# Kernel optimization log

Measured on AMD Instinct MI355X. Metric: run time of the kernel, lower is better.

Reference implementation:

```python
import jax, jax.numpy as jnp
import numpy as np
import math

B, S, HID = 2, 2048, 2048
NH, NKV, HD = 16, 4, 128
ROPE_BASE = 10000.0

def _rope(x, position_ids):
    # x: [B, H, S, HD], position_ids: [B, S]
    half = HD // 2
    inv_freq = 1.0 / (ROPE_BASE ** (jnp.arange(0, half, dtype=jnp.float32) / half))
    freqs = position_ids.astype(jnp.float32)[:, :, None] * inv_freq[None, None, :]  # [B,S,half]
    cos = jnp.cos(freqs)[:, None, :, :]  # [B,1,S,half]
    sin = jnp.sin(freqs)[:, None, :, :]
    x1, x2 = x[..., :half], x[..., half:]
    return jnp.concatenate([x1 * cos - x2 * sin, x2 * cos + x1 * sin], axis=-1)

def setup_inputs() -> dict:
    key = jax.random.key(0)
    k1, k2, k3 = jax.random.split(key, 3)
    x = jax.random.normal(k1, (B, S, HID), dtype=jnp.float32)
    position_ids = jnp.broadcast_to(jnp.arange(S, dtype=jnp.int64 if jax.config.jax_enable_x64 else jnp.int32)[None, :], (B, S))
    causal = jnp.tril(jnp.ones((S, S), dtype=bool))
    mask = jnp.where(causal, 0.0, -1e9).astype(jnp.float32)[None, None, :, :]
    w_qkv = jax.random.normal(k2, (NH * HD + 2 * NKV * HD, HID), dtype=jnp.float32) * 0.02
    w_o = jax.random.normal(k3, (HID, HID), dtype=jnp.float32) * 0.02
    return {"x": x, "position_ids": position_ids, "mask": mask, "w_qkv": w_qkv, "w_o": w_o}

def reference(x, position_ids, mask, w_qkv, w_o):
    qkv = x @ w_qkv.T  # [B,S,3072]
    q_dim, kv_dim = NH * HD, NKV * HD
    q = qkv[..., :q_dim].reshape(B, S, NH, HD).transpose(0, 2, 1, 3)          # [B,NH,S,HD]
    k = qkv[..., q_dim:q_dim + kv_dim].reshape(B, S, NKV, HD).transpose(0, 2, 1, 3)
    v = qkv[..., q_dim + kv_dim:].reshape(B, S, NKV, HD).transpose(0, 2, 1, 3)
    q = _rope(q, position_ids)
    k = _rope(k, position_ids)
    n_rep = NH // NKV
    k = jnp.repeat(k, n_rep, axis=1)  # [B,NH,S,HD]
    v = jnp.repeat(v, n_rep, axis=1)
    scores = jnp.einsum('bhqd,bhkd->bhqk', q, k) / math.sqrt(HD) + mask
    attn = jax.nn.softmax(scores, axis=-1)  # dropout p=0.0 -> identity
    out = jnp.einsum('bhqk,bhkd->bhqd', attn, v)
    out = out.transpose(0, 2, 1, 3).reshape(B, S, HID)
    return out @ w_o.T
```

## Files before the change

### kernel.cpp

```cpp
#include <hip/hip_runtime.h>
#include <hip/hip_bf16.h>
#include <cstdint>
#include <cstddef>

typedef unsigned short u16;
typedef __attribute__((ext_vector_type(8))) __bf16 bf16x8;
typedef __attribute__((ext_vector_type(4))) float floatx4;

#define B_    2
#define S_    2048
#define HID_  2048
#define NH_   16
#define NKV_  4
#define HD_   128
#define QKVN_ 3072

__device__ __forceinline__ float bf2f(u16 u) {
  union { unsigned int i; float f; } v; v.i = ((unsigned int)u) << 16; return v.f;
}
__device__ __forceinline__ u16 f2bf(float f) {
  union { float f; unsigned int i; } v; v.f = f;
  unsigned int u = v.i;
  return (u16)((u + 0x7fffu + ((u >> 16) & 1u)) >> 16);
}

#define GLOAD_LDS16(gp, lp)                                                  \
  __builtin_amdgcn_global_load_lds(                                          \
      (__attribute__((address_space(1))) void*)(gp),                         \
      (__attribute__((address_space(3))) void*)(lp), 16, 0, 0)

__global__ __launch_bounds__(256)
void cast_f32_bf16(const float* __restrict__ in, u16* __restrict__ out, int n)
{
  const int i = (blockIdx.x * 256 + threadIdx.x) * 8;
  if (i >= n) return;
  const float4 a = *(const float4*)(in + i);
  const float4 b = *(const float4*)(in + i + 4);
  union { u16 h[8]; uint4 v; } o;
  o.h[0] = f2bf(a.x); o.h[1] = f2bf(a.y); o.h[2] = f2bf(a.z); o.h[3] = f2bf(a.w);
  o.h[4] = f2bf(b.x); o.h[5] = f2bf(b.y); o.h[6] = f2bf(b.z); o.h[7] = f2bf(b.w);
  *(uint4*)(out + i) = o.v;
}

template <bool F32OUT>
__global__ __launch_bounds__(256, 2)
void gemm_bt_128(const u16* __restrict__ A, const u16* __restrict__ W,
                 void* __restrict__ Cv, int N, int K, int lda, int ldc)
{
  __shared__ __align__(16) u16 lA[128 * 64];
  __shared__ __align__(16) u16 lB[128 * 64];
  const int tid  = threadIdx.x;
  const int w    = tid >> 6, ln = tid & 63;
  const int quad = ln >> 4,  l15 = ln & 15;
  const int m0 = blockIdx.y * 128, n0 = blockIdx.x * 128;
  const int waveM = (w >> 1) * 64, waveN = (w & 1) * 64;

  const floatx4 vzero = {0.f, 0.f, 0.f, 0.f};
  floatx4 acc[4][4];
#pragma unroll
  for (int i = 0; i < 4; ++i)
#pragma unroll
    for (int j = 0; j < 4; ++j) acc[i][j] = vzero;

  for (int k0 = 0; k0 < K; k0 += 64) {
    __syncthreads();
#pragma unroll
    for (int p = 0; p < 4; ++p) {
      const int L = (p * 4 + w) * 64 + ln;
      const int row = L >> 3, c = L & 7;
      GLOAD_LDS16(A + (size_t)(m0 + row) * lda + k0 + c * 8, lA + L * 8);
      GLOAD_LDS16(W + (size_t)(n0 + row) * K   + k0 + c * 8, lB + L * 8);
    }
    __syncthreads();
#pragma unroll
    for (int kk = 0; kk < 64; kk += 32) {
      bf16x8 aF[4], bF[4];
      const int cbase = (kk >> 3) + quad;
#pragma unroll
      for (int t = 0; t < 4; ++t) {
        const int rowA = waveM + t * 16 + l15;
        aF[t] = *(const bf16x8*)(lA + rowA * 64 + cbase * 8);
        const int rowB = waveN + t * 16 + l15;
        bF[t] = *(const bf16x8*)(lB + rowB * 64 + cbase * 8);
      }
#pragma unroll
      for (int i = 0; i < 4; ++i)
#pragma unroll
        for (int j = 0; j < 4; ++j)
          acc[i][j] = __builtin_amdgcn_mfma_f32_16x16x32_bf16(aF[i], bF[j], acc[i][j], 0, 0, 0);
    }
  }
#pragma unroll
  for (int i = 0; i < 4; ++i)
#pragma unroll
    for (int r = 0; r < 4; ++r) {
      const int row = m0 + waveM + i * 16 + quad * 4 + r;
      if (F32OUT) {
        float* cp = (float*)Cv + (size_t)row * ldc + n0 + waveN + l15;
#pragma unroll
        for (int j = 0; j < 4; ++j) cp[j * 16] = acc[i][j][r];
      } else {
        u16* cp = (u16*)Cv + (size_t)row * ldc + n0 + waveN + l15;
#pragma unroll
        for (int j = 0; j < 4; ++j) cp[j * 16] = f2bf(acc[i][j][r]);
      }
    }
}

__global__ __launch_bounds__(256)
void rope_inplace(u16* __restrict__ qkv, u16* __restrict__ vt_ws)
{
  const int s = blockIdx.x, b = blockIdx.y;
  const int tid = threadIdx.x;
  __shared__ float cs[64], sn[64];
  if (tid < 64) {
    const float inv = powf(10000.0f, -((float)tid) / 64.0f);
    float s_, c_;
    sincosf((float)s * inv, &s_, &c_);
    cs[tid] = c_; sn[tid] = s_;
  }
  __syncthreads();
  u16* base = qkv + ((size_t)b * S_ + s) * QKVN_;
  for (int p = tid; p < NH_ * 64; p += 256) {
    const int h = p >> 6, i = p & 63;
    u16* hp = base + h * 128;
    const float x1 = bf2f(hp[i]);
    const float x2 = bf2f(hp[64 + i]);
    hp[i]      = f2bf(x1 * cs[i] - x2 * sn[i]);
    hp[64 + i] = f2bf(x2 * cs[i] + x1 * sn[i]);
  }
  for (int p = tid; p < NKV_ * 64; p += 256) {
    const int h = p >> 6, i = p & 63;
    u16* hp = base + NH_ * HD_ + h * 128;
    const float x1 = bf2f(hp[i]);
    const float x2 = bf2f(hp[64 + i]);
    hp[i]      = f2bf(x1 * cs[i] - x2 * sn[i]);
    hp[64 + i] = f2bf(x2 * cs[i] + x1 * sn[i]);
  }
  for (int p = tid; p < NKV_ * HD_; p += 256) {
    const int h = p >> 7, d = p & 127;
    vt_ws[((size_t)(b * NKV_ + h) * HD_ + d) * S_ + s] =
        base[NH_ * HD_ + NKV_ * HD_ + h * 128 + d];
  }
}

#define LKP  136
#define LVP  72
__global__ __launch_bounds__(256, 2)
void flash_attn(u16* __restrict__ qkv, const u16* __restrict__ vt_ws)
{
  const int pi = blockIdx.x;
  const int h  = blockIdx.y;
  const int b  = blockIdx.z;
  const int tid  = threadIdx.x;
  const int w    = tid >> 6, ln = tid & 63;
  const int quad = ln >> 4,  l15 = ln & 15;
  const int kvh  = h >> 2;

  __shared__ __align__(16) u16 lK[64 * LKP];
  __shared__ __align__(16) u16 lVt[128 * LVP];
  __shared__ __align__(16) u16 lP[4][16 * LVP];

  const float scale = 0.08838834764831845f;
  const u16* kbase = qkv + (size_t)b * S_ * QKVN_ + NH_ * HD_ + kvh * HD_;
  const u16* vbase = vt_ws + (size_t)(b * NKV_ + kvh) * HD_ * S_;
  const floatx4 vzero = {0.f, 0.f, 0.f, 0.f};

#pragma unroll 1
  for (int half = 0; half < 2; ++half) {
    const int qt = half ? (31 - pi) : pi;
    const int qrow0 = qt * 64 + w * 16;

    bf16x8 qF[4];
    {
      const u16* qp = qkv + ((size_t)(b * S_) + qrow0 + l15) * QKVN_ + h * HD_;
#pragma unroll
      for (int c = 0; c < 4; ++c)
        qF[c] = *(const bf16x8*)(qp + c * 32 + quad * 8);
    }

    float m_i[4], l_i[4];
    floatx4 Oacc[8];
#pragma unroll
    for (int r = 0; r < 4; ++r) { m_i[r] = -1e30f; l_i[r] = 0.f; }
#pragma unroll
    for (int t = 0; t < 8; ++t) Oacc[t] = vzero;

    const int ktEnd = qt + 1;
#pragma unroll 1
    for (int kt = 0; kt < ktEnd; ++kt) {
      __syncthreads();
#pragma unroll
      for (int p = 0; p < 4; ++p) {
        const int idx = p * 256 + tid;
        const int key = idx >> 4, cslot = idx & 15;
        *(uint4*)(lK + key * LKP + cslot * 8) =
            *(const uint4*)(kbase + (size_t)(kt * 64 + key) * QKVN_ + cslot * 8);
        const int d = idx >> 3, c2 = idx & 7;
        *(uint4*)(lVt + d * LVP + c2 * 8) =
            *(const uint4*)(vbase + (size_t)d * S_ + kt * 64 + c2 * 8);
      }
      __syncthreads();

      floatx4 sc[4];
#pragma unroll
      for (int nt = 0; nt < 4; ++nt) {
        floatx4 a = vzero;
        const int keyloc = nt * 16 + l15;
#pragma unroll
        for (int c = 0; c < 4; ++c) {
          const bf16x8 kF = *(const bf16x8*)(lK + keyloc * LKP + (c * 4 + quad) * 8);
          a = __builtin_amdgcn_mfma_f32_16x16x32_bf16(qF[c], kF, a, 0, 0, 0);
        }
        sc[nt] = a;
      }

      float pr[4][4];
#pragma unroll
      for (int r = 0; r < 4; ++r) {
        const int qrow = qrow0 + quad * 4 + r;
        float s[4];
#pragma unroll
        for (int nt = 0; nt < 4; ++nt) {
          const int key0 = kt * 64 + nt * 16 + l15;
          s[nt] = sc[nt][r] * scale + ((key0 <= qrow) ? 0.f : -1e9f);
        }
        float mx = fmaxf(fmaxf(s[0], s[1]), fmaxf(s[2], s[3]));
#pragma unroll
        for (int off = 1; off < 16; off <<= 1) mx = fmaxf(mx, __shfl_xor(mx, off, 64));
        const float mn = fmaxf(m_i[r], mx);
        const float alpha = __expf(m_i[r] - mn);
        float sm = 0.f;
#pragma unroll
        for (int nt = 0; nt < 4; ++nt) {
          const float p = __expf(s[nt] - mn);
          pr[nt][r] = p;
          sm += p;
        }
#pragma unroll
        for (int off = 1; off < 16; off <<= 1) sm += __shfl_xor(sm, off, 64);
        l_i[r] = l_i[r] * alpha + sm;
        m_i[r] = mn;
#pragma unroll
        for (int t = 0; t < 8; ++t) Oacc[t][r] *= alpha;
      }

#pragma unroll
      for (int nt = 0; nt < 4; ++nt)
#pragma unroll
        for (int r = 0; r < 4; ++r)
          lP[w][(quad * 4 + r) * LVP + nt * 16 + l15] = f2bf(pr[nt][r]);
      __syncthreads();

      {
        const bf16x8 pF0 = *(const bf16x8*)(&lP[w][l15 * LVP + quad * 8]);
        const bf16x8 pF1 = *(const bf16x8*)(&lP[w][l15 * LVP + 32 + quad * 8]);
#pragma unroll
        for (int t = 0; t < 8; ++t) {
          const int d = t * 16 + l15;
          const bf16x8 vF0 = *(const bf16x8*)(lVt + d * LVP + quad * 8);
          const bf16x8 vF1 = *(const bf16x8*)(lVt + d * LVP + 32 + quad * 8);
          Oacc[t] = __builtin_amdgcn_mfma_f32_16x16x32_bf16(pF0, vF0, Oacc[t], 0, 0, 0);
          Oacc[t] = __builtin_amdgcn_mfma_f32_16x16x32_bf16(pF1, vF1, Oacc[t], 0, 0, 0);
        }
      }
    }

#pragma unroll
    for (int r = 0; r < 4; ++r) l_i[r] = 1.0f / l_i[r];
#pragma unroll
    for (int t = 0; t < 8; ++t) {
      const int d = t * 16 + l15;
#pragma unroll
      for (int r = 0; r < 4; ++r) {
        const int qrow = qrow0 + quad * 4 + r;
        qkv[((size_t)(b * S_ + qrow)) * QKVN_ + h * HD_ + d] = f2bf(Oacc[t][r] * l_i[r]);
      }
    }
  }
}

extern "C" void kernel_launch(void* const* d_in, const int* in_sizes, int n_in,
                              void* d_out, int out_size, void* d_ws, size_t ws_size,
                              hipStream_t stream)
{
  (void)in_sizes; (void)n_in; (void)out_size; (void)ws_size;
  const float* x     = (const float*)d_in[0];
  const float* w_qkv = (const float*)d_in[3];
  const float* w_o   = (const float*)d_in[4];
  float* out = (float*)d_out;

  const int nX  = B_ * S_ * HID_;
  const int nWq = QKVN_ * HID_;
  const int nWo = HID_ * HID_;

  u16* ws    = (u16*)d_ws;
  u16* qkv   = ws;
  u16* slotW = qkv + (size_t)(B_ * S_) * QKVN_;
  u16* xb    = (u16*)d_out;
  u16* vt_ws = (u16*)d_out;

  const dim3 blk(256);
  cast_f32_bf16<<<nX  / 2048, blk, 0, stream>>>(x,     xb,    nX);
  cast_f32_bf16<<<nWq / 2048, blk, 0, stream>>>(w_qkv, slotW, nWq);
  gemm_bt_128<false><<<dim3(QKVN_ / 128, (B_ * S_) / 128), blk, 0, stream>>>(
      xb, slotW, qkv, QKVN_, HID_, HID_, QKVN_);
  rope_inplace<<<dim3(S_, B_), blk, 0, stream>>>(qkv, vt_ws);
  cast_f32_bf16<<<nWo / 2048, blk, 0, stream>>>(w_o, slotW, nWo);
  flash_attn<<<dim3(16, NH_, B_), blk, 0, stream>>>(qkv, vt_ws);
  gemm_bt_128<true><<<dim3(HID_ / 128, (B_ * S_) / 128), blk, 0, stream>>>(
      qkv, slotW, out, HID_, HID_, QKVN_, HID_);
}
```

Baseline: 405.8 us.

## Prefetch next K/V tile into registers and give each block a single query tile

The flash attention kernel now loads the next K and V tiles into registers while the current tile's MFMAs run, then writes them to shared memory after a barrier. This hides global load latency and removes one barrier per iteration, since the per-wave lP buffer no longer needs a block-wide sync. The paired query-tile scheme (pi and 31-pi) is replaced by one tile per block over a 32-wide grid ordered heaviest first. Launch bounds are raised to 3 blocks per CU. The extra prefetch registers under the tighter occupancy bound risk spills.

```diff
diff --git a/kernel.cpp b/kernel.cpp
--- a/kernel.cpp
+++ b/kernel.cpp
@@ -146,10 +146,10 @@
 
 #define LKP  136
 #define LVP  72
-__global__ __launch_bounds__(256, 2)
+__global__ __launch_bounds__(256, 3)
 void flash_attn(u16* __restrict__ qkv, const u16* __restrict__ vt_ws)
 {
-  const int pi = blockIdx.x;
+  const int qt = 31 - (int)blockIdx.x;
   const int h  = blockIdx.y;
   const int b  = blockIdx.z;
   const int tid  = threadIdx.x;
@@ -166,116 +166,137 @@
   const u16* vbase = vt_ws + (size_t)(b * NKV_ + kvh) * HD_ * S_;
   const floatx4 vzero = {0.f, 0.f, 0.f, 0.f};
 
+  const int qrow0 = qt * 64 + w * 16;
+
+  bf16x8 qF[4];
+  {
+    const u16* qp = qkv + ((size_t)(b * S_) + qrow0 + l15) * QKVN_ + h * HD_;
+#pragma unroll
+    for (int c = 0; c < 4; ++c)
+      qF[c] = *(const bf16x8*)(qp + c * 32 + quad * 8);
+  }
+
+  float m_i[4], l_i[4];
+  floatx4 Oacc[8];
+#pragma unroll
+  for (int r = 0; r < 4; ++r) { m_i[r] = -1e30f; l_i[r] = 0.f; }
+#pragma unroll
+  for (int t = 0; t < 8; ++t) Oacc[t] = vzero;
+
+  uint4 kReg[4], vReg[4];
+
+#pragma unroll
+  for (int p = 0; p < 4; ++p) {
+    const int idx = p * 256 + tid;
+    kReg[p] = *(const uint4*)(kbase + (size_t)(idx >> 4) * QKVN_ + (idx & 15) * 8);
+    vReg[p] = *(const uint4*)(vbase + (size_t)(idx >> 3) * S_ + (idx & 7) * 8);
+  }
+#pragma unroll
+  for (int p = 0; p < 4; ++p) {
+    const int idx = p * 256 + tid;
+    *(uint4*)(lK  + (idx >> 4) * LKP + (idx & 15) * 8) = kReg[p];
+    *(uint4*)(lVt + (idx >> 3) * LVP + (idx &  7) * 8) = vReg[p];
+  }
+  __syncthreads();
+
+  const int ktEnd = qt + 1;
 #pragma unroll 1
-  for (int half = 0; half < 2; ++half) {
-    const int qt = half ? (31 - pi) : pi;
-    const int qrow0 = qt * 64 + w * 16;
-
-    bf16x8 qF[4];
-    {
-      const u16* qp = qkv + ((size_t)(b * S_) + qrow0 + l15) * QKVN_ + h * HD_;
-#pragma unroll
-      for (int c = 0; c < 4; ++c)
-        qF[c] = *(const bf16x8*)(qp + c * 32 + quad * 8);
-    }
-
-    float m_i[4], l_i[4];
-    floatx4 Oacc[8];
-#pragma unroll
-    for (int r = 0; r < 4; ++r) { m_i[r] = -1e30f; l_i[r] = 0.f; }
-#pragma unroll
-    for (int t = 0; t < 8; ++t) Oacc[t] = vzero;
-
-    const int ktEnd = qt + 1;
-#pragma unroll 1
-    for (int kt = 0; kt < ktEnd; ++kt) {
-      __syncthreads();
+  for (int kt = 0; kt < ktEnd; ++kt) {
+    const bool pf = (kt + 1 < ktEnd);
+    if (pf) {
 #pragma unroll
       for (int p = 0; p < 4; ++p) {
         const int idx = p * 256 + tid;
-        const int key = idx >> 4, cslot = idx & 15;
-        *(uint4*)(lK + key * LKP + cslot * 8) =
-            *(const uint4*)(kbase + (size_t)(kt * 64 + key) * QKVN_ + cslot * 8);
-        const int d = idx >> 3, c2 = idx & 7;
-        *(uint4*)(lVt + d * LVP + c2 * 8) =
-            *(const uint4*)(vbase + (size_t)d * S_ + kt * 64 + c2 * 8);
+        kReg[p] = *(const uint4*)(kbase +
+            (size_t)((kt + 1) * 64 + (idx >> 4)) * QKVN_ + (idx & 15) * 8);
+        vReg[p] = *(const uint4*)(vbase +
+            (size_t)(idx >> 3) * S_ + (kt + 1) * 64 + (idx & 7) * 8);
+      }
+    }
+
+    floatx4 sc[4];
+#pragma unroll
+    for (int nt = 0; nt < 4; ++nt) {
+      floatx4 a = vzero;
+      const int keyloc = nt * 16 + l15;
+#pragma unroll
+      for (int c = 0; c < 4; ++c) {
+        const bf16x8 kF = *(const bf16x8*)(lK + keyloc * LKP + (c * 4 + quad) * 8);
+        a = __builtin_amdgcn_mfma_f32_16x16x32_bf16(qF[c], kF, a, 0, 0, 0);
+      }
+      sc[nt] = a;
+    }
+
+    float pr[4][4];
+#pragma unroll
+    for (int r = 0; r < 4; ++r) {
+      const int qrow = qrow0 + quad * 4 + r;
+      float s[4];
+#pragma unroll
+      for (int nt = 0; nt < 4; ++nt) {
+        const int key0 = kt * 64 + nt * 16 + l15;
+        s[nt] = sc[nt][r] * scale + ((key0 <= qrow) ? 0.f : -1e9f);
+      }
+      float mx = fmaxf(fmaxf(s[0], s[1]), fmaxf(s[2], s[3]));
+#pragma unroll
+      for (int off = 1; off < 16; off <<= 1) mx = fmaxf(mx, __shfl_xor(mx, off, 64));
+      const float mn = fmaxf(m_i[r], mx);
+      const float alpha = __expf(m_i[r] - mn);
+      float sm = 0.f;
+#pragma unroll
+      for (int nt = 0; nt < 4; ++nt) {
+        const float p = __expf(s[nt] - mn);
+        pr[nt][r] = p;
+        sm += p;
+      }
+#pragma unroll
+      for (int off = 1; off < 16; off <<= 1) sm += __shfl_xor(sm, off, 64);
+      l_i[r] = l_i[r] * alpha + sm;
+      m_i[r] = mn;
+#pragma unroll
+      for (int t = 0; t < 8; ++t) Oacc[t][r] *= alpha;
+    }
+
+#pragma unroll
+    for (int nt = 0; nt < 4; ++nt)
+#pragma unroll
+      for (int r = 0; r < 4; ++r)
+        lP[w][(quad * 4 + r) * LVP + nt * 16 + l15] = f2bf(pr[nt][r]);
+
+    {
+      const bf16x8 pF0 = *(const bf16x8*)(&lP[w][l15 * LVP + quad * 8]);
+      const bf16x8 pF1 = *(const bf16x8*)(&lP[w][l15 * LVP + 32 + quad * 8]);
+#pragma unroll
+      for (int t = 0; t < 8; ++t) {
+        const int d = t * 16 + l15;
+        const bf16x8 vF0 = *(const bf16x8*)(lVt + d * LVP + quad * 8);
+        const bf16x8 vF1 = *(const bf16x8*)(lVt + d * LVP + 32 + quad * 8);
+        Oacc[t] = __builtin_amdgcn_mfma_f32_16x16x32_bf16(pF0, vF0, Oacc[t], 0, 0, 0);
+        Oacc[t] = __builtin_amdgcn_mfma_f32_16x16x32_bf16(pF1, vF1, Oacc[t], 0, 0, 0);
+      }
+    }
+
+    __syncthreads();
+    if (pf) {
+#pragma unroll
+      for (int p = 0; p < 4; ++p) {
+        const int idx = p * 256 + tid;
+        *(uint4*)(lK  + (idx >> 4) * LKP + (idx & 15) * 8) = kReg[p];
+        *(uint4*)(lVt + (idx >> 3) * LVP + (idx &  7) * 8) = vReg[p];
       }
       __syncthreads();
-
-      floatx4 sc[4];
-#pragma unroll
-      for (int nt = 0; nt < 4; ++nt) {
-        floatx4 a = vzero;
-        const int keyloc = nt * 16 + l15;
-#pragma unroll
-        for (int c = 0; c < 4; ++c) {
-          const bf16x8 kF = *(const bf16x8*)(lK + keyloc * LKP + (c * 4 + quad) * 8);
-          a = __builtin_amdgcn_mfma_f32_16x16x32_bf16(qF[c], kF, a, 0, 0, 0);
-        }
-        sc[nt] = a;
-      }
-
-      float pr[4][4];
-#pragma unroll
-      for (int r = 0; r < 4; ++r) {
-        const int qrow = qrow0 + quad * 4 + r;
-        float s[4];
-#pragma unroll
-        for (int nt = 0; nt < 4; ++nt) {
-          const int key0 = kt * 64 + nt * 16 + l15;
-          s[nt] = sc[nt][r] * scale + ((key0 <= qrow) ? 0.f : -1e9f);
-        }
-        float mx = fmaxf(fmaxf(s[0], s[1]), fmaxf(s[2], s[3]));
-#pragma unroll
-        for (int off = 1; off < 16; off <<= 1) mx = fmaxf(mx, __shfl_xor(mx, off, 64));
-        const float mn = fmaxf(m_i[r], mx);
-        const float alpha = __expf(m_i[r] - mn);
-        float sm = 0.f;
-#pragma unroll
-        for (int nt = 0; nt < 4; ++nt) {
-          const float p = __expf(s[nt] - mn);
-          pr[nt][r] = p;
-          sm += p;
-        }
-#pragma unroll
-        for (int off = 1; off < 16; off <<= 1) sm += __shfl_xor(sm, off, 64);
-        l_i[r] = l_i[r] * alpha + sm;
-        m_i[r] = mn;
-#pragma unroll
-        for (int t = 0; t < 8; ++t) Oacc[t][r] *= alpha;
-      }
-
-#pragma unroll
-      for (int nt = 0; nt < 4; ++nt)
-#pragma unroll
-        for (int r = 0; r < 4; ++r)
-          lP[w][(quad * 4 + r) * LVP + nt * 16 + l15] = f2bf(pr[nt][r]);
-      __syncthreads();
-
-      {
-        const bf16x8 pF0 = *(const bf16x8*)(&lP[w][l15 * LVP + quad * 8]);
-        const bf16x8 pF1 = *(const bf16x8*)(&lP[w][l15 * LVP + 32 + quad * 8]);
-#pragma unroll
-        for (int t = 0; t < 8; ++t) {
-          const int d = t * 16 + l15;
-          const bf16x8 vF0 = *(const bf16x8*)(lVt + d * LVP + quad * 8);
-          const bf16x8 vF1 = *(const bf16x8*)(lVt + d * LVP + 32 + quad * 8);
-          Oacc[t] = __builtin_amdgcn_mfma_f32_16x16x32_bf16(pF0, vF0, Oacc[t], 0, 0, 0);
-          Oacc[t] = __builtin_amdgcn_mfma_f32_16x16x32_bf16(pF1, vF1, Oacc[t], 0, 0, 0);
-        }
-      }
-    }
-
-#pragma unroll
-    for (int r = 0; r < 4; ++r) l_i[r] = 1.0f / l_i[r];
-#pragma unroll
-    for (int t = 0; t < 8; ++t) {
-      const int d = t * 16 + l15;
-#pragma unroll
-      for (int r = 0; r < 4; ++r) {
-        const int qrow = qrow0 + quad * 4 + r;
-        qkv[((size_t)(b * S_ + qrow)) * QKVN_ + h * HD_ + d] = f2bf(Oacc[t][r] * l_i[r]);
-      }
+    }
+  }
+
+#pragma unroll
+  for (int r = 0; r < 4; ++r) l_i[r] = 1.0f / l_i[r];
+#pragma unroll
+  for (int t = 0; t < 8; ++t) {
+    const int d = t * 16 + l15;
+#pragma unroll
+    for (int r = 0; r < 4; ++r) {
+      const int qrow = qrow0 + quad * 4 + r;
+      qkv[((size_t)(b * S_ + qrow)) * QKVN_ + h * HD_ + d] = f2bf(Oacc[t][r] * l_i[r]);
     }
   }
 }
@@ -307,7 +328,7 @@
       xb, slotW, qkv, QKVN_, HID_, HID_, QKVN_);
   rope_inplace<<<dim3(S_, B_), blk, 0, stream>>>(qkv, vt_ws);
   cast_f32_bf16<<<nWo / 2048, blk, 0, stream>>>(w_o, slotW, nWo);
-  flash_attn<<<dim3(16, NH_, B_), blk, 0, stream>>>(qkv, vt_ws);
+  flash_attn<<<dim3(32, NH_, B_), blk, 0, stream>>>(qkv, vt_ws);
   gemm_bt_128<true><<<dim3(HID_ / 128, (B_ * S_) / 128), blk, 0, stream>>>(
       qkv, slotW, out, HID_, HID_, QKVN_, HID_);
 }
```

Result: slower. 557.4 us (+37.3%).

## Double-buffer K/V tiles with direct global-to-LDS loads and XOR swizzle

Applied to the files above, without the earlier changes.

The flash attention kernel now double-buffers K and V^T tiles in LDS and prefetches the next tile with direct global-to-LDS loads (GLOAD_LDS16) while computing the current one. Padding is replaced by an XOR swizzle to avoid bank conflicts. The paired causal q-tile scheme becomes one q-tile per block, with 32 blocks along x, largest tiles first. The aim is to hide global load latency and cut barrier stalls, at the cost of more LDS per block (which may limit occupancy) and the loss of built-in causal load balancing.

```diff
diff --git a/kernel.cpp b/kernel.cpp
--- a/kernel.cpp
+++ b/kernel.cpp
@@ -144,12 +144,14 @@
   }
 }
 
-#define LKP  136
-#define LVP  72
+#define LPP 68
+#define KSLOT(key, s) ((key) * 128 + (((s) ^ ((key) & 7)) * 8))
+#define VSLOT(d, s)   ((d) * 64  + (((s) ^ ((d) & 7)) * 8))
+
 __global__ __launch_bounds__(256, 2)
 void flash_attn(u16* __restrict__ qkv, const u16* __restrict__ vt_ws)
 {
-  const int pi = blockIdx.x;
+  const int qt = 31 - (int)blockIdx.x;
   const int h  = blockIdx.y;
   const int b  = blockIdx.z;
   const int tid  = threadIdx.x;
@@ -157,125 +159,143 @@
   const int quad = ln >> 4,  l15 = ln & 15;
   const int kvh  = h >> 2;
 
-  __shared__ __align__(16) u16 lK[64 * LKP];
-  __shared__ __align__(16) u16 lVt[128 * LVP];
-  __shared__ __align__(16) u16 lP[4][16 * LVP];
+  __shared__ __align__(16) u16 lK[2][64 * 128];
+  __shared__ __align__(16) u16 lVt[2][128 * 64];
+  __shared__ __align__(16) u16 lP[4][16 * LPP];
 
   const float scale = 0.08838834764831845f;
   const u16* kbase = qkv + (size_t)b * S_ * QKVN_ + NH_ * HD_ + kvh * HD_;
   const u16* vbase = vt_ws + (size_t)(b * NKV_ + kvh) * HD_ * S_;
   const floatx4 vzero = {0.f, 0.f, 0.f, 0.f};
 
+  const int qrow0 = qt * 64 + w * 16;
+
+  bf16x8 qF[4];
+  {
+    const u16* qp = qkv + ((size_t)(b * S_) + qrow0 + l15) * QKVN_ + h * HD_;
+#pragma unroll
+    for (int c = 0; c < 4; ++c)
+      qF[c] = *(const bf16x8*)(qp + c * 32 + quad * 8);
+  }
+
+  float m_i[4], l_i[4];
+  floatx4 Oacc[8];
+#pragma unroll
+  for (int r = 0; r < 4; ++r) { m_i[r] = -1e30f; l_i[r] = 0.f; }
+#pragma unroll
+  for (int t = 0; t < 8; ++t) Oacc[t] = vzero;
+
+#pragma unroll
+  for (int p = 0; p < 4; ++p) {
+    const int idx = (w * 4 + p) * 64 + ln;
+    const int key = idx >> 4, ks = idx & 15;
+    GLOAD_LDS16(kbase + (size_t)key * QKVN_ + ((ks ^ (key & 7)) * 8),
+                lK[0] + (w * 4 + p) * 512);
+    const int d = idx >> 3, vs = idx & 7;
+    GLOAD_LDS16(vbase + (size_t)d * S_ + ((vs ^ (d & 7)) * 8),
+                lVt[0] + (w * 4 + p) * 512);
+  }
+
+  const int ktEnd = qt + 1;
 #pragma unroll 1
-  for (int half = 0; half < 2; ++half) {
-    const int qt = half ? (31 - pi) : pi;
-    const int qrow0 = qt * 64 + w * 16;
-
-    bf16x8 qF[4];
+  for (int kt = 0; kt < ktEnd; ++kt) {
+    const u16* lKc = lK[kt & 1];
+    const u16* lVc = lVt[kt & 1];
+    const bool pf = (kt + 1 < ktEnd);
+    if (pf) {
+      u16* lKn = lK[(kt + 1) & 1];
+      u16* lVn = lVt[(kt + 1) & 1];
+#pragma unroll
+      for (int p = 0; p < 4; ++p) {
+        const int idx = (w * 4 + p) * 64 + ln;
+        const int key = idx >> 4, ks = idx & 15;
+        GLOAD_LDS16(kbase + (size_t)((kt + 1) * 64 + key) * QKVN_ + ((ks ^ (key & 7)) * 8),
+                    lKn + (w * 4 + p) * 512);
+        const int d = idx >> 3, vs = idx & 7;
+        GLOAD_LDS16(vbase + (size_t)d * S_ + (kt + 1) * 64 + ((vs ^ (d & 7)) * 8),
+                    lVn + (w * 4 + p) * 512);
+      }
+      asm volatile("s_waitcnt vmcnt(8)" ::: "memory");
+    } else {
+      asm volatile("s_waitcnt vmcnt(0)" ::: "memory");
+    }
+    __builtin_amdgcn_s_barrier();
+    __builtin_amdgcn_sched_barrier(0);
+
+    floatx4 sc[4];
+#pragma unroll
+    for (int nt = 0; nt < 4; ++nt) {
+      floatx4 a = vzero;
+      const int keyloc = nt * 16 + l15;
+#pragma unroll
+      for (int c = 0; c < 4; ++c) {
+        const bf16x8 kF = *(const bf16x8*)(lKc + KSLOT(keyloc, c * 4 + quad));
+        a = __builtin_amdgcn_mfma_f32_16x16x32_bf16(qF[c], kF, a, 0, 0, 0);
+      }
+      sc[nt] = a;
+    }
+
+    float pr[4][4];
+#pragma unroll
+    for (int r = 0; r < 4; ++r) {
+      const int qrow = qrow0 + quad * 4 + r;
+      float s[4];
+#pragma unroll
+      for (int nt = 0; nt < 4; ++nt) {
+        const int key0 = kt * 64 + nt * 16 + l15;
+        s[nt] = sc[nt][r] * scale + ((key0 <= qrow) ? 0.f : -1e9f);
+      }
+      float mx = fmaxf(fmaxf(s[0], s[1]), fmaxf(s[2], s[3]));
+#pragma unroll
+      for (int off = 1; off < 16; off <<= 1) mx = fmaxf(mx, __shfl_xor(mx, off, 64));
+      const float mn = fmaxf(m_i[r], mx);
+      const float alpha = __expf(m_i[r] - mn);
+      float sm = 0.f;
+#pragma unroll
+      for (int nt = 0; nt < 4; ++nt) {
+        const float p = __expf(s[nt] - mn);
+        pr[nt][r] = p;
+        sm += p;
+      }
+#pragma unroll
+      for (int off = 1; off < 16; off <<= 1) sm += __shfl_xor(sm, off, 64);
+      l_i[r] = l_i[r] * alpha + sm;
+      m_i[r] = mn;
+#pragma unroll
+      for (int t = 0; t < 8; ++t) Oacc[t][r] *= alpha;
+    }
+
+#pragma unroll
+    for (int nt = 0; nt < 4; ++nt)
+#pragma unroll
+      for (int r = 0; r < 4; ++r)
+        lP[w][(quad * 4 + r) * LPP + nt * 16 + l15] = f2bf(pr[nt][r]);
+
     {
-      const u16* qp = qkv + ((size_t)(b * S_) + qrow0 + l15) * QKVN_ + h * HD_;
-#pragma unroll
-      for (int c = 0; c < 4; ++c)
-        qF[c] = *(const bf16x8*)(qp + c * 32 + quad * 8);
-    }
-
-    float m_i[4], l_i[4];
-    floatx4 Oacc[8];
-#pragma unroll
-    for (int r = 0; r < 4; ++r) { m_i[r] = -1e30f; l_i[r] = 0.f; }
-#pragma unroll
-    for (int t = 0; t < 8; ++t) Oacc[t] = vzero;
-
-    const int ktEnd = qt + 1;
-#pragma unroll 1
-    for (int kt = 0; kt < ktEnd; ++kt) {
-      __syncthreads();
-#pragma unroll
-      for (int p = 0; p < 4; ++p) {
-        const int idx = p * 256 + tid;
-        const int key = idx >> 4, cslot = idx & 15;
-        *(uint4*)(lK + key * LKP + cslot * 8) =
-            *(const uint4*)(kbase + (size_t)(kt * 64 + key) * QKVN_ + cslot * 8);
-        const int d = idx >> 3, c2 = idx & 7;
-        *(uint4*)(lVt + d * LVP + c2 * 8) =
-            *(const uint4*)(vbase + (size_t)d * S_ + kt * 64 + c2 * 8);
-      }
-      __syncthreads();
-
-      floatx4 sc[4];
-#pragma unroll
-      for (int nt = 0; nt < 4; ++nt) {
-        floatx4 a = vzero;
-        const int keyloc = nt * 16 + l15;
-#pragma unroll
-        for (int c = 0; c < 4; ++c) {
-          const bf16x8 kF = *(const bf16x8*)(lK + keyloc * LKP + (c * 4 + quad) * 8);
-          a = __builtin_amdgcn_mfma_f32_16x16x32_bf16(qF[c], kF, a, 0, 0, 0);
-        }
-        sc[nt] = a;
-      }
-
-      float pr[4][4];
-#pragma unroll
-      for (int r = 0; r < 4; ++r) {
-        const int qrow = qrow0 + quad * 4 + r;
-        float s[4];
-#pragma unroll
-        for (int nt = 0; nt < 4; ++nt) {
-          const int key0 = kt * 64 + nt * 16 + l15;
-          s[nt] = sc[nt][r] * scale + ((key0 <= qrow) ? 0.f : -1e9f);
-        }
-        float mx = fmaxf(fmaxf(s[0], s[1]), fmaxf(s[2], s[3]));
-#pragma unroll
-        for (int off = 1; off < 16; off <<= 1) mx = fmaxf(mx, __shfl_xor(mx, off, 64));
-        const float mn = fmaxf(m_i[r], mx);
-        const float alpha = __expf(m_i[r] - mn);
-        float sm = 0.f;
-#pragma unroll
-        for (int nt = 0; nt < 4; ++nt) {
-          const float p = __expf(s[nt] - mn);
-          pr[nt][r] = p;
-          sm += p;
-        }
-#pragma unroll
-        for (int off = 1; off < 16; off <<= 1) sm += __shfl_xor(sm, off, 64);
-        l_i[r] = l_i[r] * alpha + sm;
-        m_i[r] = mn;
-#pragma unroll
-        for (int t = 0; t < 8; ++t) Oacc[t][r] *= alpha;
-      }
-
-#pragma unroll
-      for (int nt = 0; nt < 4; ++nt)
-#pragma unroll
-        for (int r = 0; r < 4; ++r)
-          lP[w][(quad * 4 + r) * LVP + nt * 16 + l15] = f2bf(pr[nt][r]);
-      __syncthreads();
-
-      {
-        const bf16x8 pF0 = *(const bf16x8*)(&lP[w][l15 * LVP + quad * 8]);
-        const bf16x8 pF1 = *(const bf16x8*)(&lP[w][l15 * LVP + 32 + quad * 8]);
-#pragma unroll
-        for (int t = 0; t < 8; ++t) {
-          const int d = t * 16 + l15;
-          const bf16x8 vF0 = *(const bf16x8*)(lVt + d * LVP + quad * 8);
-          const bf16x8 vF1 = *(const bf16x8*)(lVt + d * LVP + 32 + quad * 8);
-          Oacc[t] = __builtin_amdgcn_mfma_f32_16x16x32_bf16(pF0, vF0, Oacc[t], 0, 0, 0);
-          Oacc[t] = __builtin_amdgcn_mfma_f32_16x16x32_bf16(pF1, vF1, Oacc[t], 0, 0, 0);
-        }
-      }
-    }
-
-#pragma unroll
-    for (int r = 0; r < 4; ++r) l_i[r] = 1.0f / l_i[r];
-#pragma unroll
-    for (int t = 0; t < 8; ++t) {
-      const int d = t * 16 + l15;
-#pragma unroll
-      for (int r = 0; r < 4; ++r) {
-        const int qrow = qrow0 + quad * 4 + r;
-        qkv[((size_t)(b * S_ + qrow)) * QKVN_ + h * HD_ + d] = f2bf(Oacc[t][r] * l_i[r]);
-      }
+      const bf16x8 pF0 = *(const bf16x8*)(&lP[w][l15 * LPP + quad * 8]);
+      const bf16x8 pF1 = *(const bf16x8*)(&lP[w][l15 * LPP + 32 + quad * 8]);
+#pragma unroll
+      for (int t = 0; t < 8; ++t) {
+        const int d = t * 16 + l15;
+        const bf16x8 vF0 = *(const bf16x8*)(lVc + VSLOT(d, quad));
+        const bf16x8 vF1 = *(const bf16x8*)(lVc + VSLOT(d, 4 + quad));
+        Oacc[t] = __builtin_amdgcn_mfma_f32_16x16x32_bf16(pF0, vF0, Oacc[t], 0, 0, 0);
+        Oacc[t] = __builtin_amdgcn_mfma_f32_16x16x32_bf16(pF1, vF1, Oacc[t], 0, 0, 0);
+      }
+    }
+
+    __builtin_amdgcn_s_barrier();
+  }
+
+#pragma unroll
+  for (int r = 0; r < 4; ++r) l_i[r] = 1.0f / l_i[r];
+#pragma unroll
+  for (int t = 0; t < 8; ++t) {
+    const int d = t * 16 + l15;
+#pragma unroll
+    for (int r = 0; r < 4; ++r) {
+      const int qrow = qrow0 + quad * 4 + r;
+      qkv[((size_t)(b * S_ + qrow)) * QKVN_ + h * HD_ + d] = f2bf(Oacc[t][r] * l_i[r]);
     }
   }
 }
@@ -307,7 +327,7 @@
       xb, slotW, qkv, QKVN_, HID_, HID_, QKVN_);
   rope_inplace<<<dim3(S_, B_), blk, 0, stream>>>(qkv, vt_ws);
   cast_f32_bf16<<<nWo / 2048, blk, 0, stream>>>(w_o, slotW, nWo);
-  flash_attn<<<dim3(16, NH_, B_), blk, 0, stream>>>(qkv, vt_ws);
+  flash_attn<<<dim3(32, NH_, B_), blk, 0, stream>>>(qkv, vt_ws);
   gemm_bt_128<true><<<dim3(HID_ / 128, (B_ * S_) / 128), blk, 0, stream>>>(
       qkv, slotW, out, HID_, HID_, QKVN_, HID_);
 }
```

After: 420.3 us. 1.04x slower.
